# Kernel tuning notes

Measured on AMD Instinct MI355X. Metric: run time of the kernel, lower is better.

The kernel has to match this reference:

```python
import jax, jax.numpy as jnp
import numpy as np

B, S, E = 8, 1024, 512      # batch, seq, emb_size
L, H, K, F = 2, 4, 4, 128    # blocks, heads, conv kernel, final_size
I = 2 * E                    # inner dim (proj_factor=2)
DH = I // H                  # head dim
EPS = 1e-5


def _layernorm(x, g, b):
    mu = jnp.mean(x, axis=-1, keepdims=True)
    var = jnp.var(x, axis=-1, keepdims=True)
    return (x - mu) * jax.lax.rsqrt(var + EPS) * g + b


def _causal_conv(x, w, b):
    # x: [B,S,I], w: [K,I] depthwise, left-padded causal conv
    y = jax.lax.conv_general_dilated(
        x, w[:, None, :], window_strides=(1,), padding=[(K - 1, 0)],
        dimension_numbers=('NWC', 'WIO', 'NWC'), feature_group_count=I)
    return y + b


def _mlstm_parallel(q, k, v, ipre, fpre):
    # q,k,v: [B,H,S,DH]; ipre,fpre: [B,H,S]  (stabilized parallel mLSTM)
    lf = jax.nn.log_sigmoid(fpre)                       # [B,H,S]
    lfc = jnp.cumsum(lf, axis=-1)
    logD = lfc[..., :, None] - lfc[..., None, :] + ipre[..., None, :]  # [B,H,S,S]
    mask = jnp.tril(jnp.ones((S, S), dtype=bool))
    logD = jnp.where(mask, logD, -jnp.inf)
    m = jnp.max(logD, axis=-1, keepdims=True)           # [B,H,S,1]
    Dm = jnp.exp(logD - m)
    scores = jnp.einsum('bhtd,bhsd->bhts', q, k) * (DH ** -0.5) * Dm
    n = jnp.maximum(jnp.abs(jnp.sum(scores, axis=-1, keepdims=True)), jnp.exp(-m))
    return jnp.einsum('bhts,bhsd->bhtd', scores, v) / n


def _block(x, ln_g, ln_b, w_up, conv_w, conv_b, wq, wk, wv,
           w_i, b_i, w_f, b_f, skip, gn_g, w_down, b_down):
    res = x
    xn = _layernorm(x, ln_g, ln_b)
    up = xn @ w_up                                      # [B,S,2I]
    x_m, z = up[..., :I], up[..., I:]
    c_act = jax.nn.silu(_causal_conv(x_m, conv_w, conv_b))
    q = c_act @ wq
    k = c_act @ wk
    v = x_m @ wv
    qkv = jnp.concatenate([q, k, v], axis=-1)           # [B,S,3I]
    ipre = jnp.transpose(qkv @ w_i + b_i, (0, 2, 1))    # [B,H,S]
    fpre = jnp.transpose(qkv @ w_f + b_f, (0, 2, 1))
    to_h = lambda t: jnp.transpose(t.reshape(B, S, H, DH), (0, 2, 1, 3))
    h = _mlstm_parallel(to_h(q), to_h(k), to_h(v), ipre, fpre)  # [B,H,S,DH]
    # per-head group norm
    mu = jnp.mean(h, axis=-1, keepdims=True)
    var = jnp.var(h, axis=-1, keepdims=True)
    h = (h - mu) * jax.lax.rsqrt(var + EPS)
    h = jnp.transpose(h, (0, 2, 1, 3)).reshape(B, S, I) * gn_g
    h = h + skip * c_act
    h = h * jax.nn.silu(z)
    return res + h @ w_down + b_down


def setup_inputs() -> dict:
    key = jax.random.key(0)
    ks = jax.random.split(key, 12)
    n = lambda k, shp, s=0.02: jax.random.normal(k, shp, jnp.float32) * s
    return {
        'x': jax.random.normal(ks[0], (B, S, E), jnp.float32),
        'ln_g': jnp.ones((L, E), jnp.float32), 'ln_b': jnp.zeros((L, E), jnp.float32),
        'w_up': n(ks[1], (L, E, 2 * I)),
        'conv_w': n(ks[2], (L, K, I), 0.1), 'conv_b': jnp.zeros((L, I), jnp.float32),
        'wq': n(ks[3], (L, I, I)), 'wk': n(ks[4], (L, I, I)), 'wv': n(ks[5], (L, I, I)),
        'w_i': n(ks[6], (L, 3 * I, H)), 'b_i': jnp.zeros((L, H), jnp.float32),
        'w_f': n(ks[7], (L, 3 * I, H)), 'b_f': 3.0 * jnp.ones((L, H), jnp.float32),
        'skip': jnp.ones((L, I), jnp.float32), 'gn_g': jnp.ones((L, I), jnp.float32),
        'w_down': n(ks[8], (L, I, E)), 'b_down': jnp.zeros((L, E), jnp.float32),
        'w_fin': n(ks[9], (E, F)), 'b_fin': jnp.zeros((F,), jnp.float32),
    }


def reference(x, ln_g, ln_b, w_up, conv_w, conv_b, wq, wk, wv, w_i, b_i,
              w_f, b_f, skip, gn_g, w_down, b_down, w_fin, b_fin):
    h = x
    for l in range(L):  # 2 structurally identical mLSTM blocks
        h = _block(h, ln_g[l], ln_b[l], w_up[l], conv_w[l], conv_b[l],
                   wq[l], wk[l], wv[l], w_i[l], b_i[l], w_f[l], b_f[l],
                   skip[l], gn_g[l], w_down[l], b_down[l])
    return h @ w_fin + b_fin
```

## Files before the change

kernel.cpp:

```cpp
#include <hip/hip_runtime.h>
#include <math.h>

#define S_LEN 1024
#define I_DIM 1024
#define DH_   256
#define H_NUM 4
#define B_NUM 8
#define ROWS  (B_NUM*S_LEN)

#define GLOBAL_AS __attribute__((address_space(1)))
#define LDS_AS    __attribute__((address_space(3)))

typedef __attribute__((ext_vector_type(8))) short bf16x8;
typedef __attribute__((ext_vector_type(4))) float f32x4;
typedef unsigned short u16;

__device__ __forceinline__ u16 f2bf(float f) {
    union { float f; unsigned u; } v; v.f = f;
    unsigned r = v.u + 0x7FFF + ((v.u >> 16) & 1);
    return (u16)(r >> 16);
}
__device__ __forceinline__ float bf2f(u16 h) {
    union { unsigned u; float f; } v; v.u = ((unsigned)h) << 16;
    return v.f;
}

__global__ __launch_bounds__(64) void ln_fused_k(const float* __restrict__ x,
                                                 const float* __restrict__ g,
                                                 const float* __restrict__ b,
                                                 u16* __restrict__ out) {
    int row = blockIdx.x, lane = threadIdx.x;
    const float* xr = x + (size_t)row * 512;
    float4 a = *(const float4*)&xr[lane * 8];
    float4 c = *(const float4*)&xr[lane * 8 + 4];
    float s  = a.x + a.y + a.z + a.w + c.x + c.y + c.z + c.w;
    float s2 = a.x*a.x + a.y*a.y + a.z*a.z + a.w*a.w
             + c.x*c.x + c.y*c.y + c.z*c.z + c.w*c.w;
#pragma unroll
    for (int off = 32; off > 0; off >>= 1) {
        s  += __shfl_down(s, off);
        s2 += __shfl_down(s2, off);
    }
    s = __shfl(s, 0); s2 = __shfl(s2, 0);
    float mu = s * (1.f / 512.f);
    float rstd = rsqrtf(s2 * (1.f / 512.f) - mu * mu + 1e-5f);
    int e0 = lane * 8;
    float y[8] = {a.x,a.y,a.z,a.w,c.x,c.y,c.z,c.w};
    ushort4 o0, o1;
    o0.x = f2bf((y[0]-mu)*rstd*g[e0+0]+b[e0+0]);
    o0.y = f2bf((y[1]-mu)*rstd*g[e0+1]+b[e0+1]);
    o0.z = f2bf((y[2]-mu)*rstd*g[e0+2]+b[e0+2]);
    o0.w = f2bf((y[3]-mu)*rstd*g[e0+3]+b[e0+3]);
    o1.x = f2bf((y[4]-mu)*rstd*g[e0+4]+b[e0+4]);
    o1.y = f2bf((y[5]-mu)*rstd*g[e0+5]+b[e0+5]);
    o1.z = f2bf((y[6]-mu)*rstd*g[e0+6]+b[e0+6]);
    o1.w = f2bf((y[7]-mu)*rstd*g[e0+7]+b[e0+7]);
    *(ushort4*)&out[(size_t)row * 512 + e0]     = o0;
    *(ushort4*)&out[(size_t)row * 512 + e0 + 4] = o1;
}

__global__ __launch_bounds__(256) void cvtT_k(const float* __restrict__ W,
                                              u16* __restrict__ Wt, int K, int N) {
    __shared__ float t[32][33];
    int k0 = blockIdx.x * 32, n0 = blockIdx.y * 32;
    int c = threadIdx.x & 31, r8 = threadIdx.x >> 5;
#pragma unroll
    for (int q = 0; q < 4; q++) {
        int r = r8 * 4 + q;
        t[r][c] = W[(size_t)(k0 + r) * N + n0 + c];
    }
    __syncthreads();
#pragma unroll
    for (int q = 0; q < 4; q++) {
        int r = r8 * 4 + q;
        Wt[(size_t)(n0 + r) * K + k0 + c] = f2bf(t[c][r]);
    }
}

__global__ __launch_bounds__(256) void vt_k(const u16* __restrict__ v,
                                            u16* __restrict__ vt) {
    __shared__ u16 t[32][34];
    int s0 = blockIdx.x * 32, d0 = blockIdx.y * 32, bh = blockIdx.z;
    int b = bh >> 2, h = bh & 3;
    int c = threadIdx.x & 31, r4 = threadIdx.x >> 5;
#pragma unroll
    for (int q = 0; q < 4; q++) {
        int r = r4 * 4 + q;
        t[r][c] = v[(size_t)(b * 1024 + s0 + r) * I_DIM + h * 256 + d0 + c];
    }
    __syncthreads();
#pragma unroll
    for (int q = 0; q < 4; q++) {
        int r = r4 * 4 + q;
        vt[((size_t)bh * 256 + d0 + r) * 1024 + s0 + c] = t[c][r];
    }
}

template<int EPI>
__global__ __launch_bounds__(256) void gemm_bf16_k(
    const u16* __restrict__ A, const u16* __restrict__ Wt, int N, int K,
    float* __restrict__ Cf, u16* __restrict__ Cb,
    const float* __restrict__ bias, const float* __restrict__ res, int ldres)
{
    __shared__ __align__(16) u16 As[128 * 32];
    __shared__ __align__(16) u16 Bs[128 * 32];
    int tid = threadIdx.x;
    int lane = tid & 63;
    int wm = (tid >> 6) & 1, wn = tid >> 7;
    int r0 = blockIdx.y * 128, n0 = blockIdx.x * 128;
    int arow = tid >> 2, acol = (tid & 3) * 8;
    const u16* ap0 = A  + (size_t)(r0 + arow) * K + acol;
    const u16* ap1 = A  + (size_t)(r0 + 64 + arow) * K + acol;
    const u16* bp0 = Wt + (size_t)(n0 + arow) * K + acol;
    const u16* bp1 = Wt + (size_t)(n0 + 64 + arow) * K + acol;
    u16* al0 = As + tid * 8;
    u16* al1 = As + 2048 + tid * 8;
    u16* bl0 = Bs + tid * 8;
    u16* bl1 = Bs + 2048 + tid * 8;

    f32x4 acc[4][4];
#pragma unroll
    for (int i = 0; i < 4; i++)
#pragma unroll
        for (int j = 0; j < 4; j++) acc[i][j] = (f32x4){0.f, 0.f, 0.f, 0.f};

    int lm = lane & 15, lk = (lane >> 4) * 8;
    for (int k0 = 0; k0 < K; k0 += 32) {
        __builtin_amdgcn_global_load_lds((const GLOBAL_AS unsigned int*)(ap0 + k0), (LDS_AS unsigned int*)al0, 16, 0, 0);
        __builtin_amdgcn_global_load_lds((const GLOBAL_AS unsigned int*)(ap1 + k0), (LDS_AS unsigned int*)al1, 16, 0, 0);
        __builtin_amdgcn_global_load_lds((const GLOBAL_AS unsigned int*)(bp0 + k0), (LDS_AS unsigned int*)bl0, 16, 0, 0);
        __builtin_amdgcn_global_load_lds((const GLOBAL_AS unsigned int*)(bp1 + k0), (LDS_AS unsigned int*)bl1, 16, 0, 0);
        __syncthreads();
        bf16x8 af[4], bfr[4];
#pragma unroll
        for (int f = 0; f < 4; f++) {
            af[f]  = *(const bf16x8*)&As[(wm * 64 + f * 16 + lm) * 32 + lk];
            bfr[f] = *(const bf16x8*)&Bs[(wn * 64 + f * 16 + lm) * 32 + lk];
        }
#pragma unroll
        for (int i = 0; i < 4; i++)
#pragma unroll
            for (int j = 0; j < 4; j++)
                acc[i][j] = __builtin_amdgcn_mfma_f32_16x16x32_bf16(af[i], bfr[j], acc[i][j], 0, 0, 0);
        __syncthreads();
    }
    int lr = (lane >> 4) * 4;
#pragma unroll
    for (int i = 0; i < 4; i++) {
#pragma unroll
        for (int j = 0; j < 4; j++) {
#pragma unroll
            for (int q = 0; q < 4; q++) {
                int row = r0 + wm * 64 + i * 16 + lr + q;
                int col = n0 + wn * 64 + j * 16 + lm;
                float o = acc[i][j][q];
                if (EPI == 0) {
                    Cb[(size_t)row * N + col] = f2bf(o);
                } else if (EPI == 1) {
                    if (col < 1024) Cb[(size_t)row * 1024 + col] = f2bf(o);
                    else            Cf[(size_t)row * 1024 + (col - 1024)] = o;
                } else if (EPI == 2) {
                    o += bias[col] + res[(size_t)row * ldres + col];
                    Cf[(size_t)row * N + col] = o;
                    Cb[(size_t)row * N + col] = f2bf(o);
                } else {
                    o += bias[col];
                    Cf[(size_t)row * N + col] = o;
                }
            }
        }
    }
}

__global__ __launch_bounds__(256) void conv_k(const u16* __restrict__ xm,
                                              const float* __restrict__ w,
                                              const float* __restrict__ cb,
                                              u16* __restrict__ cact) {
    int idx = blockIdx.x * 256 + threadIdx.x;
    int r = idx >> 8;
    int c = (idx & 255) * 4;
    int t = r & 1023;
    const u16* base = xm + (size_t)(r - t) * I_DIM;
    float4 acc = *(const float4*)&cb[c];
#pragma unroll
    for (int j = 0; j < 4; j++) {
        int tt = t - 3 + j;
        if (tt >= 0) {
            short4 s = *(const short4*)&base[(size_t)tt * I_DIM + c];
            float4 wv = *(const float4*)&w[j * I_DIM + c];
            acc.x = fmaf(bf2f((u16)s.x), wv.x, acc.x);
            acc.y = fmaf(bf2f((u16)s.y), wv.y, acc.y);
            acc.z = fmaf(bf2f((u16)s.z), wv.z, acc.z);
            acc.w = fmaf(bf2f((u16)s.w), wv.w, acc.w);
        }
    }
    acc.x = acc.x / (1.f + __expf(-acc.x));
    acc.y = acc.y / (1.f + __expf(-acc.y));
    acc.z = acc.z / (1.f + __expf(-acc.z));
    acc.w = acc.w / (1.f + __expf(-acc.w));
    ushort4 o;
    o.x = f2bf(acc.x); o.y = f2bf(acc.y); o.z = f2bf(acc.z); o.w = f2bf(acc.w);
    *(ushort4*)&cact[(size_t)r * I_DIM + c] = o;
}

__global__ __launch_bounds__(256) void gates_k(const u16* __restrict__ q,
                                               const u16* __restrict__ k,
                                               const u16* __restrict__ v,
                                               const float* __restrict__ wi,
                                               const float* __restrict__ bi,
                                               const float* __restrict__ wf,
                                               const float* __restrict__ bf,
                                               float* __restrict__ ipre,
                                               float* __restrict__ fpre) {
    int r = blockIdx.x;
    int tid = threadIdx.x;
    float ai[4] = {0,0,0,0}, af[4] = {0,0,0,0};
#pragma unroll
    for (int part = 0; part < 3; part++) {
        const u16* src = (part == 0 ? q : (part == 1 ? k : v)) + (size_t)r * I_DIM;
        const float* wip = wi + part * I_DIM * 4;
        const float* wfp = wf + part * I_DIM * 4;
#pragma unroll
        for (int jj = 0; jj < 4; jj++) {
            int e = tid + jj * 256;
            float xv = bf2f(src[e]);
            float4 w4 = *(const float4*)&wip[e * 4];
            ai[0] = fmaf(xv, w4.x, ai[0]);
            ai[1] = fmaf(xv, w4.y, ai[1]);
            ai[2] = fmaf(xv, w4.z, ai[2]);
            ai[3] = fmaf(xv, w4.w, ai[3]);
            float4 f4v = *(const float4*)&wfp[e * 4];
            af[0] = fmaf(xv, f4v.x, af[0]);
            af[1] = fmaf(xv, f4v.y, af[1]);
            af[2] = fmaf(xv, f4v.z, af[2]);
            af[3] = fmaf(xv, f4v.w, af[3]);
        }
    }
#pragma unroll
    for (int off = 32; off > 0; off >>= 1) {
#pragma unroll
        for (int m = 0; m < 4; m++) {
            ai[m] += __shfl_down(ai[m], off);
            af[m] += __shfl_down(af[m], off);
        }
    }
    __shared__ float red[4][8];
    int wv_ = tid >> 6, lane = tid & 63;
    if (lane == 0) {
#pragma unroll
        for (int m = 0; m < 4; m++) { red[wv_][m] = ai[m]; red[wv_][4 + m] = af[m]; }
    }
    __syncthreads();
    if (tid < 8) {
        float s_ = red[0][tid] + red[1][tid] + red[2][tid] + red[3][tid];
        int b = r >> 10, ss = r & 1023;
        if (tid < 4) ipre[((size_t)(b * 4 + tid)) * 1024 + ss] = s_ + bi[tid];
        else         fpre[((size_t)(b * 4 + (tid - 4))) * 1024 + ss] = s_ + bf[tid - 4];
    }
}

__global__ __launch_bounds__(1024) void scan_k(const float* __restrict__ ipre,
                                               const float* __restrict__ fpre,
                                               float* __restrict__ cA,
                                               float* __restrict__ MA,
                                               float* __restrict__ nF) {
    __shared__ float buf[1024];
    int bh = blockIdx.x, t = threadIdx.x;
    size_t base = (size_t)bh * 1024;
    float fp = fpre[base + t];
    float lf = (fp >= 0.f) ? -log1pf(expf(-fp)) : (fp - log1pf(expf(fp)));
    buf[t] = lf; __syncthreads();
    for (int off = 1; off < 1024; off <<= 1) {
        float u = (t >= off) ? buf[t - off] : 0.f;
        __syncthreads();
        buf[t] += u;
        __syncthreads();
    }
    float lfc = buf[t];
    float c = ipre[base + t] - lfc;
    __syncthreads();
    buf[t] = c; __syncthreads();
    for (int off = 1; off < 1024; off <<= 1) {
        float u = (t >= off) ? buf[t - off] : -3.4e38f;
        __syncthreads();
        buf[t] = fmaxf(buf[t], u);
        __syncthreads();
    }
    float M = buf[t];
    cA[base + t] = c * 1.44269504f;
    MA[base + t] = M * 1.44269504f;
    nF[base + t] = expf(-(lfc + M));
}

__global__ __launch_bounds__(256) void attn_k(
    const u16* __restrict__ qg, const u16* __restrict__ kg, const u16* __restrict__ vt,
    const float* __restrict__ c2A, const float* __restrict__ M2A, const float* __restrict__ nFl,
    const u16* __restrict__ cact, const float* __restrict__ zb, u16* __restrict__ hb,
    const float* __restrict__ gng, const float* __restrict__ skip)
{
    __shared__ __align__(16) u16 Kb[2][32 * 256];
    __shared__ __align__(16) u16 Vb[2][256 * 32];
    __shared__ __align__(16) u16 Ps[64 * 40];
    __shared__ float rsI[64];
    __shared__ float gS[64 * 4];
    __shared__ float gQ[64 * 4];
    __shared__ float gmu[64], gvr[64];

    int tid = threadIdx.x;
    int w = tid >> 6, l = tid & 63;
    int lm = l & 15, lk = l >> 4;
    int b = blockIdx.z, h = blockIdx.y;
    int T0 = blockIdx.x * 64;
    int bh32 = b * H_NUM + h;
    size_t bh = (size_t)bh32 * S_LEN;

    bf16x8 qf[8];
    {
        size_t base = ((size_t)(b * S_LEN + T0 + w * 16 + lm)) * I_DIM + h * DH_ + lk * 8;
#pragma unroll
        for (int ks = 0; ks < 8; ks++) qf[ks] = *(const bf16x8*)&qg[base + ks * 32];
    }
    f32x4 acc[4][4];
#pragma unroll
    for (int i = 0; i < 4; i++)
#pragma unroll
        for (int jd = 0; jd < 4; jd++) acc[i][jd] = (f32x4){0.f, 0.f, 0.f, 0.f};
    float rsum[2][4] = {{0,0,0,0},{0,0,0,0}};
    float m2r[4]; int tg[4];
#pragma unroll
    for (int q = 0; q < 4; q++) {
        tg[q] = T0 + w * 16 + lk * 4 + q;
        m2r[q] = M2A[bh + tg[q]];
    }

    const size_t krow0 = ((size_t)(b * S_LEN)) * I_DIM + h * DH_;
    const size_t vrow0 = (size_t)bh32 * 256 * S_LEN;

    auto stage = [&](int s0, int bs) {
#pragma unroll
        for (int r = 0; r < 4; r++) {
            int q = r * 256 + tid;
            int row = q >> 5, cl = q & 31;
            int cs = cl ^ (row & 7);
            const u16* src = kg + krow0 + (size_t)(s0 + row) * I_DIM + cs * 8;
            __builtin_amdgcn_global_load_lds((const GLOBAL_AS unsigned int*)src,
                                             (LDS_AS unsigned int*)&Kb[bs][q * 8], 16, 0, 0);
        }
#pragma unroll
        for (int r = 0; r < 4; r++) {
            int q = r * 256 + tid;
            int dpair = q >> 3, cp = q & 7;
            int u = cp ^ (dpair & 7);
            int d = dpair * 2 + (u >> 2), c = u & 3;
            const u16* src = vt + vrow0 + (size_t)d * S_LEN + s0 + c * 8;
            __builtin_amdgcn_global_load_lds((const GLOBAL_AS unsigned int*)src,
                                             (LDS_AS unsigned int*)&Vb[bs][q * 8], 16, 0, 0);
        }
    };

    int nst = (T0 >> 5) + 2;
    stage(0, 0);
    for (int st = 0; st < nst; st++) {
        int s0 = st * 32;
        int cur = st & 1;
        __syncthreads();
        f32x4 sacc[2];
        sacc[0] = (f32x4){0.f,0.f,0.f,0.f};
        sacc[1] = (f32x4){0.f,0.f,0.f,0.f};
#pragma unroll
        for (int ks = 0; ks < 8; ks++) {
#pragma unroll
            for (int js = 0; js < 2; js++) {
                int row = js * 16 + lm;
                int ch = (ks * 4 + lk) ^ (row & 7);
                bf16x8 kf = *(const bf16x8*)&Kb[cur][row * 256 + ch * 8];
                sacc[js] = __builtin_amdgcn_mfma_f32_16x16x32_bf16(qf[ks], kf, sacc[js], 0, 0, 0);
            }
        }
#pragma unroll
        for (int js = 0; js < 2; js++) {
            int sg = s0 + js * 16 + lm;
            float c2 = c2A[bh + sg];
#pragma unroll
            for (int q = 0; q < 4; q++) {
                float v = sacc[js][q] * 0.0625f * exp2f(c2 - m2r[q]);
                v = (sg <= tg[q]) ? v : 0.f;
                u16 pb = f2bf(v);
                rsum[js][q] += bf2f(pb);
                Ps[(w * 16 + lk * 4 + q) * 40 + js * 16 + lm] = pb;
            }
        }
        __syncthreads();
        if (st + 1 < nst) stage(s0 + 32, cur ^ 1);
        bf16x8 vf[4];
#pragma unroll
        for (int jd = 0; jd < 4; jd++) {
            int d = w * 64 + jd * 16 + lm;
            int cp = (((d & 1) << 2) + lk) ^ ((d >> 1) & 7);
            vf[jd] = *(const bf16x8*)&Vb[cur][((d >> 1) * 8 + cp) * 8];
        }
#pragma unroll
        for (int i = 0; i < 4; i++) {
            bf16x8 pa = *(const bf16x8*)&Ps[(i * 16 + lm) * 40 + lk * 8];
#pragma unroll
            for (int jd = 0; jd < 4; jd++)
                acc[i][jd] = __builtin_amdgcn_mfma_f32_16x16x32_bf16(pa, vf[jd], acc[i][jd], 0, 0, 0);
        }
    }
    {
        float rq[4];
#pragma unroll
        for (int q = 0; q < 4; q++) rq[q] = rsum[0][q] + rsum[1][q];
#pragma unroll
        for (int m = 1; m < 16; m <<= 1) {
#pragma unroll
            for (int q = 0; q < 4; q++) rq[q] += __shfl_xor(rq[q], m);
        }
        if (lm == 0) {
#pragma unroll
            for (int q = 0; q < 4; q++) rsI[w * 16 + lk * 4 + q] = rq[q];
        }
    }
    __syncthreads();
    if (tid < 64) {
        float n = fmaxf(fabsf(rsI[tid]), nFl[bh + T0 + tid]);
        rsI[tid] = 1.f / n;
    }
    __syncthreads();
#pragma unroll
    for (int i = 0; i < 4; i++) {
#pragma unroll
        for (int q = 0; q < 4; q++) {
            int rl = i * 16 + lk * 4 + q;
            float inv = rsI[rl];
            float ps = 0.f, pq = 0.f;
#pragma unroll
            for (int jd = 0; jd < 4; jd++) {
                float v = acc[i][jd][q] * inv;
                acc[i][jd][q] = v;
                ps += v; pq += v * v;
            }
#pragma unroll
            for (int m = 1; m < 16; m <<= 1) {
                ps += __shfl_xor(ps, m);
                pq += __shfl_xor(pq, m);
            }
            if (lm == 0) { gS[rl * 4 + w] = ps; gQ[rl * 4 + w] = pq; }
        }
    }
    __syncthreads();
    if (tid < 64) {
        float s1 = gS[tid*4] + gS[tid*4+1] + gS[tid*4+2] + gS[tid*4+3];
        float s2 = gQ[tid*4] + gQ[tid*4+1] + gQ[tid*4+2] + gQ[tid*4+3];
        float mu = s1 * (1.f / 256.f);
        float var = s2 * (1.f / 256.f) - mu * mu;
        gmu[tid] = mu;
        gvr[tid] = rsqrtf(var + 1e-5f);
    }
    __syncthreads();
#pragma unroll
    for (int i = 0; i < 4; i++) {
#pragma unroll
        for (int q = 0; q < 4; q++) {
            int rl = i * 16 + lk * 4 + q;
            size_t r = (size_t)b * S_LEN + T0 + rl;
            float mu = gmu[rl], rv = gvr[rl];
#pragma unroll
            for (int jd = 0; jd < 4; jd++) {
                int cix = h * DH_ + w * 64 + jd * 16 + lm;
                float val = (acc[i][jd][q] - mu) * rv * gng[cix];
                float ca = bf2f(cact[r * I_DIM + cix]);
                float z = zb[r * I_DIM + cix];
                float hm = (val + skip[cix] * ca) * (z / (1.f + __expf(-z)));
                hb[r * I_DIM + cix] = f2bf(hm);
            }
        }
    }
}

extern "C" void kernel_launch(void* const* d_in, const int* in_sizes, int n_in,
                              void* d_out, int out_size, void* d_ws, size_t ws_size,
                              hipStream_t stream) {
    const float* x      = (const float*)d_in[0];
    const float* ln_g   = (const float*)d_in[1];
    const float* ln_b   = (const float*)d_in[2];
    const float* w_up   = (const float*)d_in[3];
    const float* conv_w = (const float*)d_in[4];
    const float* conv_b = (const float*)d_in[5];
    const float* wq     = (const float*)d_in[6];
    const float* wk     = (const float*)d_in[7];
    const float* wv     = (const float*)d_in[8];
    const float* w_i    = (const float*)d_in[9];
    const float* b_i    = (const float*)d_in[10];
    const float* w_f    = (const float*)d_in[11];
    const float* b_f    = (const float*)d_in[12];
    const float* skip   = (const float*)d_in[13];
    const float* gn_g   = (const float*)d_in[14];
    const float* w_down = (const float*)d_in[15];
    const float* b_down = (const float*)d_in[16];
    const float* w_fin  = (const float*)d_in[17];
    const float* b_fin  = (const float*)d_in[18];

    char* p = (char*)d_ws;
    auto alloc = [&](size_t bytes) { void* r = p; p += (bytes + 255) & ~(size_t)255; return r; };
    float* zbuf  = (float*)alloc((size_t)ROWS * 1024 * 4);
    float* xa    = (float*)alloc((size_t)ROWS * 512 * 4);
    float* xb2   = (float*)alloc((size_t)ROWS * 512 * 4);
    u16*  xln    = (u16*)alloc((size_t)ROWS * 512 * 2);
    u16*  xm     = (u16*)alloc((size_t)ROWS * 1024 * 2);
    u16*  cactb  = (u16*)alloc((size_t)ROWS * 1024 * 2);
    u16*  qbf    = (u16*)alloc((size_t)ROWS * 1024 * 2);
    u16*  kbf    = (u16*)alloc((size_t)ROWS * 1024 * 2);
    u16*  vbf    = (u16*)alloc((size_t)ROWS * 1024 * 2);
    u16*  vtg    = (u16*)alloc((size_t)32 * 256 * 1024 * 2);
    u16*  hbf    = (u16*)alloc((size_t)ROWS * 1024 * 2);
    u16*  xoutb  = (u16*)alloc((size_t)ROWS * 512 * 2);
    u16*  wupT   = (u16*)alloc((size_t)2 * 2048 * 512 * 2);
    u16*  wqT    = (u16*)alloc((size_t)2 * 1024 * 1024 * 2);
    u16*  wkT    = (u16*)alloc((size_t)2 * 1024 * 1024 * 2);
    u16*  wvT    = (u16*)alloc((size_t)2 * 1024 * 1024 * 2);
    u16*  wdT    = (u16*)alloc((size_t)2 * 512 * 1024 * 2);
    u16*  wfT    = (u16*)alloc((size_t)128 * 512 * 2);
    float* ipre  = (float*)alloc(32768 * 4);
    float* fpre  = (float*)alloc(32768 * 4);
    float* cA    = (float*)alloc(32768 * 4);
    float* MA    = (float*)alloc(32768 * 4);
    float* nF    = (float*)alloc(32768 * 4);

    for (int l = 0; l < 2; l++) {
        cvtT_k<<<dim3(16, 64), 256, 0, stream>>>(w_up + (size_t)l * 512 * 2048, wupT + (size_t)l * 2048 * 512, 512, 2048);
        cvtT_k<<<dim3(32, 32), 256, 0, stream>>>(wq + (size_t)l * 1024 * 1024, wqT + (size_t)l * 1024 * 1024, 1024, 1024);
        cvtT_k<<<dim3(32, 32), 256, 0, stream>>>(wk + (size_t)l * 1024 * 1024, wkT + (size_t)l * 1024 * 1024, 1024, 1024);
        cvtT_k<<<dim3(32, 32), 256, 0, stream>>>(wv + (size_t)l * 1024 * 1024, wvT + (size_t)l * 1024 * 1024, 1024, 1024);
        cvtT_k<<<dim3(32, 16), 256, 0, stream>>>(w_down + (size_t)l * 1024 * 512, wdT + (size_t)l * 512 * 1024, 1024, 512);
    }
    cvtT_k<<<dim3(16, 4), 256, 0, stream>>>(w_fin, wfT, 512, 128);

    const float* xin = x;
    for (int l = 0; l < 2; l++) {
        float* xout = (l == 0) ? xa : xb2;
        ln_fused_k<<<ROWS, 64, 0, stream>>>(xin, ln_g + l * 512, ln_b + l * 512, xln);
        gemm_bf16_k<1><<<dim3(16, 64), 256, 0, stream>>>(
            xln, wupT + (size_t)l * 2048 * 512, 2048, 512, zbuf, xm, nullptr, nullptr, 0);
        conv_k<<<ROWS, 256, 0, stream>>>(xm, conv_w + l * 4 * I_DIM, conv_b + l * I_DIM, cactb);
        gemm_bf16_k<0><<<dim3(8, 64), 256, 0, stream>>>(
            xm, wvT + (size_t)l * 1024 * 1024, 1024, 1024, nullptr, vbf, nullptr, nullptr, 0);
        gemm_bf16_k<0><<<dim3(8, 64), 256, 0, stream>>>(
            cactb, wqT + (size_t)l * 1024 * 1024, 1024, 1024, nullptr, qbf, nullptr, nullptr, 0);
        gemm_bf16_k<0><<<dim3(8, 64), 256, 0, stream>>>(
            cactb, wkT + (size_t)l * 1024 * 1024, 1024, 1024, nullptr, kbf, nullptr, nullptr, 0);
        vt_k<<<dim3(32, 8, 32), 256, 0, stream>>>(vbf, vtg);
        gates_k<<<ROWS, 256, 0, stream>>>(qbf, kbf, vbf,
            w_i + l * 3072 * 4, b_i + l * 4, w_f + l * 3072 * 4, b_f + l * 4, ipre, fpre);
        scan_k<<<32, 1024, 0, stream>>>(ipre, fpre, cA, MA, nF);
        attn_k<<<dim3(16, 4, 8), 256, 0, stream>>>(qbf, kbf, vtg, cA, MA, nF, cactb, zbuf, hbf,
            gn_g + l * I_DIM, skip + l * I_DIM);
        gemm_bf16_k<2><<<dim3(4, 64), 256, 0, stream>>>(
            hbf, wdT + (size_t)l * 512 * 1024, 512, 1024, xout, xoutb,
            b_down + l * 512, xin, 512);
        xin = xout;
    }
    gemm_bf16_k<3><<<dim3(1, 64), 256, 0, stream>>>(
        xoutb, wfT, 128, 512, (float*)d_out, nullptr, b_fin, nullptr, 0);
}
```

Baseline: 755.7 us.

## Double-buffer GEMM and attention loads, swizzle GEMM tiles, batch gate rows

The GEMM kernel gets double-buffered LDS, prefetching the next K tile with global_load_lds while MFMAs run on the current one. Workgroup IDs are remapped in groups of 8 to improve L2 locality. The attention kernel now issues its next-stage prefetch before the QK MFMAs and raises wave priority around its MFMA sections, using explicit waitcnt and barrier fences instead of __syncthreads. The gates kernel handles four rows per block so the gate weights are reused, at the cost of doubled LDS per GEMM block and more registers.

```diff
diff --git a/kernel.cpp b/kernel.cpp
--- a/kernel.cpp
+++ b/kernel.cpp
@@ -10,6 +10,11 @@
 
 #define GLOBAL_AS __attribute__((address_space(1)))
 #define LDS_AS    __attribute__((address_space(3)))
+
+#define VM0    asm volatile("s_waitcnt vmcnt(0)" ::: "memory")
+#define LGKM0  asm volatile("s_waitcnt lgkmcnt(0)" ::: "memory")
+#define BAR    __builtin_amdgcn_s_barrier()
+#define SFENCE __builtin_amdgcn_sched_barrier(0)
 
 typedef __attribute__((ext_vector_type(8))) short bf16x8;
 typedef __attribute__((ext_vector_type(4))) float f32x4;
@@ -102,21 +107,31 @@
     float* __restrict__ Cf, u16* __restrict__ Cb,
     const float* __restrict__ bias, const float* __restrict__ res, int ldres)
 {
-    __shared__ __align__(16) u16 As[128 * 32];
-    __shared__ __align__(16) u16 Bs[128 * 32];
+    __shared__ __align__(16) u16 As[2][128 * 32];
+    __shared__ __align__(16) u16 Bs[2][128 * 32];
     int tid = threadIdx.x;
     int lane = tid & 63;
     int wm = (tid >> 6) & 1, wn = tid >> 7;
-    int r0 = blockIdx.y * 128, n0 = blockIdx.x * 128;
+    int gx = gridDim.x;
+    int nwg = gx * gridDim.y;
+    int bid = blockIdx.y * gx + blockIdx.x;
+    int cpx = nwg >> 3;
+    int swz = (bid & 7) * cpx + (bid >> 3);
+    int r0 = (swz / gx) * 128, n0 = (swz % gx) * 128;
+
     int arow = tid >> 2, acol = (tid & 3) * 8;
     const u16* ap0 = A  + (size_t)(r0 + arow) * K + acol;
     const u16* ap1 = A  + (size_t)(r0 + 64 + arow) * K + acol;
     const u16* bp0 = Wt + (size_t)(n0 + arow) * K + acol;
     const u16* bp1 = Wt + (size_t)(n0 + 64 + arow) * K + acol;
-    u16* al0 = As + tid * 8;
-    u16* al1 = As + 2048 + tid * 8;
-    u16* bl0 = Bs + tid * 8;
-    u16* bl1 = Bs + 2048 + tid * 8;
+
+    auto stage = [&](int kt, int bs) {
+        int koff = kt * 32;
+        __builtin_amdgcn_global_load_lds((const GLOBAL_AS unsigned int*)(ap0 + koff), (LDS_AS unsigned int*)&As[bs][tid * 8], 16, 0, 0);
+        __builtin_amdgcn_global_load_lds((const GLOBAL_AS unsigned int*)(ap1 + koff), (LDS_AS unsigned int*)&As[bs][2048 + tid * 8], 16, 0, 0);
+        __builtin_amdgcn_global_load_lds((const GLOBAL_AS unsigned int*)(bp0 + koff), (LDS_AS unsigned int*)&Bs[bs][tid * 8], 16, 0, 0);
+        __builtin_amdgcn_global_load_lds((const GLOBAL_AS unsigned int*)(bp1 + koff), (LDS_AS unsigned int*)&Bs[bs][2048 + tid * 8], 16, 0, 0);
+    };
 
     f32x4 acc[4][4];
 #pragma unroll
@@ -125,24 +140,24 @@
         for (int j = 0; j < 4; j++) acc[i][j] = (f32x4){0.f, 0.f, 0.f, 0.f};
 
     int lm = lane & 15, lk = (lane >> 4) * 8;
-    for (int k0 = 0; k0 < K; k0 += 32) {
-        __builtin_amdgcn_global_load_lds((const GLOBAL_AS unsigned int*)(ap0 + k0), (LDS_AS unsigned int*)al0, 16, 0, 0);
-        __builtin_amdgcn_global_load_lds((const GLOBAL_AS unsigned int*)(ap1 + k0), (LDS_AS unsigned int*)al1, 16, 0, 0);
-        __builtin_amdgcn_global_load_lds((const GLOBAL_AS unsigned int*)(bp0 + k0), (LDS_AS unsigned int*)bl0, 16, 0, 0);
-        __builtin_amdgcn_global_load_lds((const GLOBAL_AS unsigned int*)(bp1 + k0), (LDS_AS unsigned int*)bl1, 16, 0, 0);
-        __syncthreads();
+    int nt = K >> 5;
+    stage(0, 0);
+    VM0; BAR; SFENCE;
+    for (int t = 0; t < nt; ++t) {
+        int cur = t & 1;
+        if (t + 1 < nt) stage(t + 1, cur ^ 1);
         bf16x8 af[4], bfr[4];
 #pragma unroll
         for (int f = 0; f < 4; f++) {
-            af[f]  = *(const bf16x8*)&As[(wm * 64 + f * 16 + lm) * 32 + lk];
-            bfr[f] = *(const bf16x8*)&Bs[(wn * 64 + f * 16 + lm) * 32 + lk];
+            af[f]  = *(const bf16x8*)&As[cur][(wm * 64 + f * 16 + lm) * 32 + lk];
+            bfr[f] = *(const bf16x8*)&Bs[cur][(wn * 64 + f * 16 + lm) * 32 + lk];
         }
 #pragma unroll
         for (int i = 0; i < 4; i++)
 #pragma unroll
             for (int j = 0; j < 4; j++)
                 acc[i][j] = __builtin_amdgcn_mfma_f32_16x16x32_bf16(af[i], bfr[j], acc[i][j], 0, 0, 0);
-        __syncthreads();
+        VM0; BAR; SFENCE;
     }
     int lr = (lane >> 4) * 4;
 #pragma unroll
@@ -212,50 +227,65 @@
                                                const float* __restrict__ bf,
                                                float* __restrict__ ipre,
                                                float* __restrict__ fpre) {
-    int r = blockIdx.x;
+    int r0 = blockIdx.x * 4;
     int tid = threadIdx.x;
-    float ai[4] = {0,0,0,0}, af[4] = {0,0,0,0};
+    float ai[4][4], af4[4][4];
+#pragma unroll
+    for (int r = 0; r < 4; r++)
+#pragma unroll
+        for (int m = 0; m < 4; m++) { ai[r][m] = 0.f; af4[r][m] = 0.f; }
 #pragma unroll
     for (int part = 0; part < 3; part++) {
-        const u16* src = (part == 0 ? q : (part == 1 ? k : v)) + (size_t)r * I_DIM;
+        const u16* src = (part == 0 ? q : (part == 1 ? k : v)) + (size_t)r0 * I_DIM;
         const float* wip = wi + part * I_DIM * 4;
         const float* wfp = wf + part * I_DIM * 4;
 #pragma unroll
         for (int jj = 0; jj < 4; jj++) {
             int e = tid + jj * 256;
-            float xv = bf2f(src[e]);
-            float4 w4 = *(const float4*)&wip[e * 4];
-            ai[0] = fmaf(xv, w4.x, ai[0]);
-            ai[1] = fmaf(xv, w4.y, ai[1]);
-            ai[2] = fmaf(xv, w4.z, ai[2]);
-            ai[3] = fmaf(xv, w4.w, ai[3]);
+            float4 w4  = *(const float4*)&wip[e * 4];
             float4 f4v = *(const float4*)&wfp[e * 4];
-            af[0] = fmaf(xv, f4v.x, af[0]);
-            af[1] = fmaf(xv, f4v.y, af[1]);
-            af[2] = fmaf(xv, f4v.z, af[2]);
-            af[3] = fmaf(xv, f4v.w, af[3]);
+#pragma unroll
+            for (int r = 0; r < 4; r++) {
+                float xv = bf2f(src[(size_t)r * I_DIM + e]);
+                ai[r][0] = fmaf(xv, w4.x, ai[r][0]);
+                ai[r][1] = fmaf(xv, w4.y, ai[r][1]);
+                ai[r][2] = fmaf(xv, w4.z, ai[r][2]);
+                ai[r][3] = fmaf(xv, w4.w, ai[r][3]);
+                af4[r][0] = fmaf(xv, f4v.x, af4[r][0]);
+                af4[r][1] = fmaf(xv, f4v.y, af4[r][1]);
+                af4[r][2] = fmaf(xv, f4v.z, af4[r][2]);
+                af4[r][3] = fmaf(xv, f4v.w, af4[r][3]);
+            }
         }
     }
 #pragma unroll
     for (int off = 32; off > 0; off >>= 1) {
 #pragma unroll
-        for (int m = 0; m < 4; m++) {
-            ai[m] += __shfl_down(ai[m], off);
-            af[m] += __shfl_down(af[m], off);
-        }
-    }
-    __shared__ float red[4][8];
+        for (int r = 0; r < 4; r++)
+#pragma unroll
+            for (int m = 0; m < 4; m++) {
+                ai[r][m]  += __shfl_down(ai[r][m], off);
+                af4[r][m] += __shfl_down(af4[r][m], off);
+            }
+    }
+    __shared__ float red[4][32];
     int wv_ = tid >> 6, lane = tid & 63;
     if (lane == 0) {
 #pragma unroll
-        for (int m = 0; m < 4; m++) { red[wv_][m] = ai[m]; red[wv_][4 + m] = af[m]; }
-    }
-    __syncthreads();
-    if (tid < 8) {
+        for (int r = 0; r < 4; r++)
+#pragma unroll
+            for (int m = 0; m < 4; m++) {
+                red[wv_][r * 8 + m]     = ai[r][m];
+                red[wv_][r * 8 + 4 + m] = af4[r][m];
+            }
+    }
+    __syncthreads();
+    if (tid < 32) {
+        int r = tid >> 3, m = tid & 7;
         float s_ = red[0][tid] + red[1][tid] + red[2][tid] + red[3][tid];
-        int b = r >> 10, ss = r & 1023;
-        if (tid < 4) ipre[((size_t)(b * 4 + tid)) * 1024 + ss] = s_ + bi[tid];
-        else         fpre[((size_t)(b * 4 + (tid - 4))) * 1024 + ss] = s_ + bf[tid - 4];
+        int row = r0 + r, bb = row >> 10, ss = row & 1023;
+        if (m < 4) ipre[((size_t)(bb * 4 + m)) * 1024 + ss] = s_ + bi[m];
+        else       fpre[((size_t)(bb * 4 + (m - 4))) * 1024 + ss] = s_ + bf[m - 4];
     }
 }
 
@@ -360,13 +390,15 @@
 
     int nst = (T0 >> 5) + 2;
     stage(0, 0);
+    VM0; BAR; SFENCE;
     for (int st = 0; st < nst; st++) {
         int s0 = st * 32;
         int cur = st & 1;
-        __syncthreads();
+        if (st + 1 < nst) stage(s0 + 32, cur ^ 1);
         f32x4 sacc[2];
         sacc[0] = (f32x4){0.f,0.f,0.f,0.f};
         sacc[1] = (f32x4){0.f,0.f,0.f,0.f};
+        __builtin_amdgcn_s_setprio(1);
 #pragma unroll
         for (int ks = 0; ks < 8; ks++) {
 #pragma unroll
@@ -377,6 +409,7 @@
                 sacc[js] = __builtin_amdgcn_mfma_f32_16x16x32_bf16(qf[ks], kf, sacc[js], 0, 0, 0);
             }
         }
+        __builtin_amdgcn_s_setprio(0);
 #pragma unroll
         for (int js = 0; js < 2; js++) {
             int sg = s0 + js * 16 + lm;
@@ -390,8 +423,7 @@
                 Ps[(w * 16 + lk * 4 + q) * 40 + js * 16 + lm] = pb;
             }
         }
-        __syncthreads();
-        if (st + 1 < nst) stage(s0 + 32, cur ^ 1);
+        LGKM0; BAR; SFENCE;
         bf16x8 vf[4];
 #pragma unroll
         for (int jd = 0; jd < 4; jd++) {
@@ -399,6 +431,7 @@
             int cp = (((d & 1) << 2) + lk) ^ ((d >> 1) & 7);
             vf[jd] = *(const bf16x8*)&Vb[cur][((d >> 1) * 8 + cp) * 8];
         }
+        __builtin_amdgcn_s_setprio(1);
 #pragma unroll
         for (int i = 0; i < 4; i++) {
             bf16x8 pa = *(const bf16x8*)&Ps[(i * 16 + lm) * 40 + lk * 8];
@@ -406,6 +439,8 @@
             for (int jd = 0; jd < 4; jd++)
                 acc[i][jd] = __builtin_amdgcn_mfma_f32_16x16x32_bf16(pa, vf[jd], acc[i][jd], 0, 0, 0);
         }
+        __builtin_amdgcn_s_setprio(0);
+        VM0; BAR; SFENCE;
     }
     {
         float rq[4];
@@ -550,7 +585,7 @@
         gemm_bf16_k<0><<<dim3(8, 64), 256, 0, stream>>>(
             cactb, wkT + (size_t)l * 1024 * 1024, 1024, 1024, nullptr, kbf, nullptr, nullptr, 0);
         vt_k<<<dim3(32, 8, 32), 256, 0, stream>>>(vbf, vtg);
-        gates_k<<<ROWS, 256, 0, stream>>>(qbf, kbf, vbf,
+        gates_k<<<ROWS / 4, 256, 0, stream>>>(qbf, kbf, vbf,
             w_i + l * 3072 * 4, b_i + l * 4, w_f + l * 3072 * 4, b_f + l * 4, ipre, fpre);
         scan_k<<<32, 1024, 0, stream>>>(ipre, fpre, cA, MA, nF);
         attn_k<<<dim3(16, 4, 8), 256, 0, stream>>>(qbf, kbf, vtg, cA, MA, nF, cactb, zbuf, hbf,
```

Result: faster. 696.5 us (-7.8%).
